# Performance work log

Measured on AMD Instinct MI355X. Metric: run time of the kernel, lower is better.

Reference implementation:

```python
import jax, jax.numpy as jnp
import numpy as np

EPS = 1e-6
DIM, HEADS, HEAD_DIM, FFN = 1024, 16, 64, 4096
B, S = 2, 2048


def layer_norm(x, g, b):
    m = jnp.mean(x, axis=-1, keepdims=True)
    v = jnp.mean(jnp.square(x - m), axis=-1, keepdims=True)
    return (x - m) * jax.lax.rsqrt(v + EPS) * g + b


def apply_rope(x, cos, sin):
    # x: (b, h, s, d); cos/sin: (s, d) broadcast over b, h
    x1, x2 = jnp.split(x, 2, axis=-1)
    rot = jnp.concatenate([-x2, x1], axis=-1)
    return x * cos + rot * sin


def setup_inputs() -> dict:
    key = jax.random.key(0)
    ks = jax.random.split(key, 24)
    sc_in = 1.0 / np.sqrt(DIM)
    sc_ffn = 1.0 / np.sqrt(FFN)
    inp = {
        "x": jax.random.normal(ks[0], (B, S, DIM), jnp.float32),
        "rope_cos": jax.random.uniform(ks[1], (S, HEAD_DIM), jnp.float32),
        "rope_sin": jax.random.uniform(ks[2], (S, HEAD_DIM), jnp.float32),
        "w_qkv": jax.random.normal(ks[3], (3 * DIM, DIM), jnp.float32) * sc_in,
        "b_qkv": jnp.zeros((3 * DIM,), jnp.float32),
        "w_out": jax.random.normal(ks[4], (DIM, DIM), jnp.float32) * sc_in,
        "b_out": jnp.zeros((DIM,), jnp.float32),
        "qn_g": jnp.ones((DIM,), jnp.float32),
        "qn_b": jnp.zeros((DIM,), jnp.float32),
        "kn_g": jnp.ones((DIM,), jnp.float32),
        "kn_b": jnp.zeros((DIM,), jnp.float32),
        "ln1_g": jnp.ones((DIM,), jnp.float32),
        "ln1_b": jnp.zeros((DIM,), jnp.float32),
        "ln2_g": jnp.ones((DIM,), jnp.float32),
        "ln2_b": jnp.zeros((DIM,), jnp.float32),
        "w1": jax.random.normal(ks[5], (FFN, DIM), jnp.float32) * sc_in,
        "b1": jnp.zeros((FFN,), jnp.float32),
        "w2": jax.random.normal(ks[6], (DIM, FFN), jnp.float32) * sc_ffn,
        "b2": jnp.zeros((DIM,), jnp.float32),
        "w3": jax.random.normal(ks[7], (FFN, DIM), jnp.float32) * sc_in,
        "b3": jnp.zeros((FFN,), jnp.float32),
    }
    return inp


def reference(x, rope_cos, rope_sin, w_qkv, b_qkv, w_out, b_out,
              qn_g, qn_b, kn_g, kn_b, ln1_g, ln1_b, ln2_g, ln2_b,
              w1, b1, w2, b2, w3, b3):
    bs, s, d = x.shape
    # --- pre-norm self-attention ---
    h = layer_norm(x, ln1_g, ln1_b)
    qkv = h @ w_qkv.T + b_qkv                      # (b, s, 3d)
    q, k, v = jnp.split(qkv, 3, axis=-1)
    q = layer_norm(q, qn_g, qn_b)                  # QK-norm over full dim
    k = layer_norm(k, kn_g, kn_b)
    # (b, s, d) -> (b, h, s, hd)
    q = q.reshape(bs, s, HEADS, HEAD_DIM).transpose(0, 2, 1, 3)
    k = k.reshape(bs, s, HEADS, HEAD_DIM).transpose(0, 2, 1, 3)
    v = v.reshape(bs, s, HEADS, HEAD_DIM).transpose(0, 2, 1, 3)
    q = apply_rope(q, rope_cos, rope_sin)
    k = apply_rope(k, rope_cos, rope_sin)
    scale = 1.0 / np.sqrt(HEAD_DIM)
    scores = jnp.einsum('bhqd,bhkd->bhqk', q, k) * scale
    probs = jax.nn.softmax(scores, axis=-1)
    attn = jnp.einsum('bhqk,bhkd->bhqd', probs, v)
    attn = attn.transpose(0, 2, 1, 3).reshape(bs, s, d)
    x = x + (attn @ w_out.T + b_out)
    # --- pre-norm SwiGLU FFN ---
    h2 = layer_norm(x, ln2_g, ln2_b)
    ffn = (jax.nn.silu(h2 @ w1.T + b1) * (h2 @ w3.T + b3)) @ w2.T + b2
    return x + ffn
```

## Files before the change

### kernel.cpp

```cpp
#include <hip/hip_runtime.h>
#include <hip/hip_bf16.h>


typedef __bf16 bf16_t;
typedef bf16_t bf16x8 __attribute__((ext_vector_type(8)));
typedef bf16_t bf16x4 __attribute__((ext_vector_type(4)));
typedef float  f32x4  __attribute__((ext_vector_type(4)));
typedef float  f32x16 __attribute__((ext_vector_type(16)));

#define DIM   1024
#define HEADS 16
#define HD    64
#define FFND  4096
#define NB    2
#define SEQ   2048
#define NTOK  (NB * SEQ)

#define GLOAD16(gp, lp) __builtin_amdgcn_global_load_lds( \
    (const __attribute__((address_space(1))) void*)(gp),  \
    (__attribute__((address_space(3))) void*)(lp), 16, 0, 0)

#define CVTPK(lo, hi_) ({ unsigned r_;                                        \
  asm("v_cvt_pk_bf16_f32 %0, %1, %2" : "=v"(r_) : "v"(lo), "v"(hi_)); r_; })
#define PLSWAP(a, b) asm("v_permlane32_swap_b32 %0, %1" : "+v"(a), "+v"(b))
#define SBAR() asm volatile("s_barrier" ::: "memory")

#define F2B_S0 786432
#define F2B_S1 262144
#define F2B_S2 1048576
#define F2B_S3 1048576
#define F2B_S4 1048576
#define F2B_C1 (F2B_S0)
#define F2B_C2 (F2B_C1 + F2B_S1)
#define F2B_C3 (F2B_C2 + F2B_S2)
#define F2B_C4 (F2B_C3 + F2B_S3)
#define F2B_N  (F2B_C4 + F2B_S4)

__global__ void f2bf_all_kernel(const float* __restrict__ s0, const float* __restrict__ s1,
                                const float* __restrict__ s2, const float* __restrict__ s3,
                                const float* __restrict__ s4,
                                bf16_t* __restrict__ d0, bf16_t* __restrict__ d1,
                                bf16_t* __restrict__ d2, bf16_t* __restrict__ d3,
                                bf16_t* __restrict__ d4) {
  int idx = blockIdx.x * blockDim.x + threadIdx.x;
  int stride = gridDim.x * blockDim.x;
  for (; idx < F2B_N; idx += stride) {
    const float* src; bf16_t* dst; int i;
    if (idx < F2B_C1)      { src = s0; dst = d0; i = idx; }
    else if (idx < F2B_C2) { src = s1; dst = d1; i = idx - F2B_C1; }
    else if (idx < F2B_C3) { src = s2; dst = d2; i = idx - F2B_C2; }
    else if (idx < F2B_C4) { src = s3; dst = d3; i = idx - F2B_C3; }
    else                   { src = s4; dst = d4; i = idx - F2B_C4; }
    float4 v = reinterpret_cast<const float4*>(src)[i];
    bf16x4 o;
    o[0] = (bf16_t)v.x; o[1] = (bf16_t)v.y; o[2] = (bf16_t)v.z; o[3] = (bf16_t)v.w;
    reinterpret_cast<bf16x4*>(dst)[i] = o;
  }
}

__global__ __launch_bounds__(256) void ln_kernel(
    const float* __restrict__ x, const float* __restrict__ g,
    const float* __restrict__ b, bf16_t* __restrict__ out) {
  int t = blockIdx.x;
  int i = threadIdx.x;
  float4 v = reinterpret_cast<const float4*>(x + (size_t)t * DIM)[i];
  float s  = v.x + v.y + v.z + v.w;
  float s2 = v.x * v.x + v.y * v.y + v.z * v.z + v.w * v.w;
#pragma unroll
  for (int off = 32; off > 0; off >>= 1) {
    s  += __shfl_down(s, off, 64);
    s2 += __shfl_down(s2, off, 64);
  }
  __shared__ float red[2][4];
  int wid = i >> 6, lane = i & 63;
  if (lane == 0) { red[0][wid] = s; red[1][wid] = s2; }
  __syncthreads();
  float S  = red[0][0] + red[0][1] + red[0][2] + red[0][3];
  float S2 = red[1][0] + red[1][1] + red[1][2] + red[1][3];
  float mean = S * (1.0f / DIM);
  float var  = S2 * (1.0f / DIM) - mean * mean;
  float r = rsqrtf(var + 1e-6f);
  float vv[4] = {v.x, v.y, v.z, v.w};
  bf16x4 o;
#pragma unroll
  for (int j = 0; j < 4; ++j) {
    int d = i * 4 + j;
    o[j] = (bf16_t)((vv[j] - mean) * r * g[d] + b[d]);
  }
  *reinterpret_cast<bf16x4*>(out + (size_t)t * DIM + i * 4) = o;
}

template <int OUT_MODE>
__global__ __launch_bounds__(512, 2) void gemm256(
    const bf16_t* __restrict__ A, const bf16_t* __restrict__ B,
    const float* __restrict__ bias, const bf16_t* __restrict__ comp,
    void* __restrict__ Cout, int M, int N, int Kfull, int Klen) {
  __shared__ __align__(16) bf16_t Al[2][256][64];
  __shared__ __align__(16) bf16_t Bl[2][256][64];
  const int nTn = N >> 8;
  const int nwg = gridDim.x;
  const int bid = blockIdx.x;
  const int swz = ((nwg & 7) == 0) ? ((bid & 7) * (nwg >> 3) + (bid >> 3)) : bid;
  const int bm = swz / nTn, bn = swz % nTn;
  const int k0base = blockIdx.z * Klen;
  const int NT = Klen >> 6;
  const int tid = threadIdx.x, wid = tid >> 6, lane = tid & 63;
  const int wm = wid >> 3, wn = wid & 3;
  const int wm2 = wid >> 2;
  (void)wm;
  const int lr = lane & 15, lg = lane >> 4;
  const int strow = wid * 8 + (lane >> 3);
  const int stg   = ((lane & 7) ^ ((lane >> 3) & 7)) << 3;
  const bf16_t* Abase = A + (size_t)(bm * 256 + strow) * Kfull + k0base + stg;
  const bf16_t* Bbase = B + (size_t)(bn * 256 + strow) * Kfull + k0base + stg;

#define STAGE_A(buf, half, c, t)                                              \
  GLOAD16(Abase + (size_t)((half) * 128 + (c) * 64) * Kfull + (t) * 64,       \
          &Al[buf][(half) * 128 + (c) * 64 + wid * 8][0])
#define STAGE_B(buf, half, c, t)                                              \
  GLOAD16(Bbase + (size_t)((half) * 128 + (c) * 64) * Kfull + (t) * 64,       \
          &Bl[buf][(half) * 128 + (c) * 64 + wid * 8][0])

  f32x4 acc[8][4] = {};
  STAGE_A(0, 0, 0, 0); STAGE_A(0, 0, 1, 0); STAGE_A(0, 1, 0, 0); STAGE_A(0, 1, 1, 0);
  STAGE_B(0, 0, 0, 0); STAGE_B(0, 0, 1, 0); STAGE_B(0, 1, 0, 0); STAGE_B(0, 1, 1, 0);

  for (int t = 0; t < NT; ++t) {
    const int cur = t & 1, nxt = cur ^ 1;
    const bool pf = (t + 1 < NT);
    if (pf) {
      STAGE_A(nxt, 0, 0, t + 1); STAGE_A(nxt, 0, 1, t + 1);
      STAGE_A(nxt, 1, 0, t + 1); STAGE_A(nxt, 1, 1, t + 1);
      asm volatile("s_waitcnt vmcnt(4)" ::: "memory");
    } else {
      asm volatile("s_waitcnt vmcnt(0)" ::: "memory");
    }
    SBAR();
    bf16x8 bfr[4][2], af[2][2];
#pragma unroll
    for (int nf = 0; nf < 4; ++nf)
#pragma unroll
      for (int ks = 0; ks < 2; ++ks) {
        const int row = wn * 64 + nf * 16 + lr;
        const int g = ((ks * 4 + lg) ^ (lane & 7)) << 3;
        bfr[nf][ks] = *reinterpret_cast<const bf16x8*>(&Bl[cur][row][g]);
      }
#pragma unroll
    for (int i = 0; i < 2; ++i)
#pragma unroll
      for (int ks = 0; ks < 2; ++ks) {
        const int row = wm2 * 128 + i * 16 + lr;
        const int g = ((ks * 4 + lg) ^ (lane & 7)) << 3;
        af[i][ks] = *reinterpret_cast<const bf16x8*>(&Al[cur][row][g]);
      }
    __builtin_amdgcn_s_setprio(1);
#pragma unroll
    for (int i = 0; i < 2; ++i)
#pragma unroll
      for (int nf = 0; nf < 4; ++nf)
#pragma unroll
        for (int ks = 0; ks < 2; ++ks)
          acc[i][nf] = __builtin_amdgcn_mfma_f32_16x16x32_bf16(af[i][ks], bfr[nf][ks], acc[i][nf], 0, 0, 0);
    __builtin_amdgcn_s_setprio(0);
    SBAR();
#pragma unroll
    for (int p = 1; p < 4; ++p) {
#pragma unroll
      for (int i = 0; i < 2; ++i)
#pragma unroll
        for (int ks = 0; ks < 2; ++ks) {
          const int row = wm2 * 128 + (p * 2 + i) * 16 + lr;
          const int g = ((ks * 4 + lg) ^ (lane & 7)) << 3;
          af[i][ks] = *reinterpret_cast<const bf16x8*>(&Al[cur][row][g]);
        }
      if (p == 1 && pf) {
        STAGE_B(nxt, 0, 0, t + 1); STAGE_B(nxt, 0, 1, t + 1);
        STAGE_B(nxt, 1, 0, t + 1); STAGE_B(nxt, 1, 1, t + 1);
      }
      SBAR();
      __builtin_amdgcn_s_setprio(1);
#pragma unroll
      for (int i = 0; i < 2; ++i)
#pragma unroll
        for (int nf = 0; nf < 4; ++nf)
#pragma unroll
          for (int ks = 0; ks < 2; ++ks)
            acc[p * 2 + i][nf] = __builtin_amdgcn_mfma_f32_16x16x32_bf16(af[i][ks], bfr[nf][ks], acc[p * 2 + i][nf], 0, 0, 0);
      __builtin_amdgcn_s_setprio(0);
      SBAR();
    }
  }
#undef STAGE_A
#undef STAGE_B
  const int r0 = lg * 4;
#pragma unroll
  for (int mf = 0; mf < 8; ++mf) {
#pragma unroll
    for (int r = 0; r < 4; ++r) {
      const int row = bm * 256 + wm2 * 128 + mf * 16 + r0 + r;
#pragma unroll
      for (int nf = 0; nf < 4; ++nf) {
        const int col = bn * 256 + wn * 64 + nf * 16 + lr;
        float v = acc[mf][nf][r];
        if (OUT_MODE == 1) {
          v += bias[col];
          reinterpret_cast<bf16_t*>(Cout)[(size_t)row * N + col] = (bf16_t)v;
        } else if (OUT_MODE == 2) {
          float* P = reinterpret_cast<float*>(Cout) + (size_t)blockIdx.z * M * N;
          P[(size_t)row * N + col] = v;
        } else {
          v += bias[col];
          float c1 = (float)comp[(size_t)row * N + col];
          float sg = c1 / (1.0f + __expf(-c1));
          reinterpret_cast<bf16_t*>(Cout)[(size_t)row * N + col] = (bf16_t)(sg * v);
        }
      }
    }
  }
}

__global__ void combine_kernel(const float* __restrict__ part,
                               const float* __restrict__ bias,
                               const float* __restrict__ res,
                               float* __restrict__ out, int n4) {
  const int slice = NTOK * DIM / 4;
  int i = blockIdx.x * blockDim.x + threadIdx.x;
  int stride = gridDim.x * blockDim.x;
  const float4* p = reinterpret_cast<const float4*>(part);
  const float4* r4 = reinterpret_cast<const float4*>(res);
  const float4* b4 = reinterpret_cast<const float4*>(bias);
  float4* o4 = reinterpret_cast<float4*>(out);
  for (; i < n4; i += stride) {
    float4 a = p[i], b = p[i + slice], c = p[i + 2 * slice], d = p[i + 3 * slice];
    float4 rr = r4[i];
    float4 bb = b4[i & 255];
    float4 o;
    o.x = a.x + b.x + c.x + d.x + bb.x + rr.x;
    o.y = a.y + b.y + c.y + d.y + bb.y + rr.y;
    o.z = a.z + b.z + c.z + d.z + bb.z + rr.z;
    o.w = a.w + b.w + c.w + d.w + bb.w + rr.w;
    o4[i] = o;
  }
}

template <int OUT_BF16, int HAS_RES>
__global__ __launch_bounds__(256) void gemm_bt(
    const bf16_t* __restrict__ A, const bf16_t* __restrict__ B,
    const float* __restrict__ bias, const float* __restrict__ res,
    void* __restrict__ Cout, int M, int N, int K) {
  __shared__ bf16_t As[128][32];
  __shared__ bf16_t Bs[128][32];
  const int nTn = N >> 7;
  const int bm = blockIdx.x / nTn;
  const int bn = blockIdx.x % nTn;
  const int tid  = threadIdx.x;
  const int wid  = tid >> 6;
  const int lane = tid & 63;
  const int wm = (wid >> 1) * 64, wn = (wid & 1) * 64;
  const int lr = lane & 15;
  const int gq = lane >> 4;
  const int sr = lane >> 2;
  const int sg = lane & 3;
  const int cS = ((sg ^ ((sr >> 1) & 3)) << 3);
  const int swg = ((gq ^ ((lr >> 1) & 3)) << 3);
  f32x4 acc[4][4] = {};
  const bf16_t* Ag0 = A + (size_t)(bm * 128 + wid * 16 + sr) * K + cS;
  const bf16_t* Ag1 = Ag0 + (size_t)64 * K;
  const bf16_t* Bg0 = B + (size_t)(bn * 128 + wid * 16 + sr) * K + cS;
  const bf16_t* Bg1 = Bg0 + (size_t)64 * K;
  bf16_t* ldsA0 = &As[wid * 16][0];
  bf16_t* ldsA1 = &As[64 + wid * 16][0];
  bf16_t* ldsB0 = &Bs[wid * 16][0];
  bf16_t* ldsB1 = &Bs[64 + wid * 16][0];
  for (int k0 = 0; k0 < K; k0 += 32) {
    __syncthreads();
    GLOAD16(Ag0 + k0, ldsA0);
    GLOAD16(Ag1 + k0, ldsA1);
    GLOAD16(Bg0 + k0, ldsB0);
    GLOAD16(Bg1 + k0, ldsB1);
    __syncthreads();
    bf16x8 af[4], bfr[4];
#pragma unroll
    for (int mi = 0; mi < 4; ++mi)
      af[mi] = *reinterpret_cast<const bf16x8*>(&As[wm + mi * 16 + lr][swg]);
#pragma unroll
    for (int ni = 0; ni < 4; ++ni)
      bfr[ni] = *reinterpret_cast<const bf16x8*>(&Bs[wn + ni * 16 + lr][swg]);
#pragma unroll
    for (int mi = 0; mi < 4; ++mi)
#pragma unroll
      for (int ni = 0; ni < 4; ++ni)
        acc[mi][ni] = __builtin_amdgcn_mfma_f32_16x16x32_bf16(af[mi], bfr[ni], acc[mi][ni], 0, 0, 0);
  }
  const int r0 = (lane >> 4) * 4;
#pragma unroll
  for (int mi = 0; mi < 4; ++mi) {
#pragma unroll
    for (int r = 0; r < 4; ++r) {
      int row = bm * 128 + wm + mi * 16 + r0 + r;
#pragma unroll
      for (int ni = 0; ni < 4; ++ni) {
        int col = bn * 128 + wn + ni * 16 + lr;
        float v = acc[mi][ni][r] + bias[col];
        if (HAS_RES) v += res[(size_t)row * N + col];
        if (OUT_BF16)
          reinterpret_cast<bf16_t*>(Cout)[(size_t)row * N + col] = (bf16_t)v;
        else
          reinterpret_cast<float*>(Cout)[(size_t)row * N + col] = v;
      }
    }
  }
}

__global__ __launch_bounds__(256) void qknorm_rope_kernel(
    const bf16_t* __restrict__ qkv,
    const float* __restrict__ qg, const float* __restrict__ qb,
    const float* __restrict__ kg, const float* __restrict__ kb,
    const float* __restrict__ rc, const float* __restrict__ rs,
    bf16_t* __restrict__ q_r, bf16_t* __restrict__ k_r) {
  int t = blockIdx.x;
  int b = t >> 11, s = t & 2047;
  const bf16_t* p = qkv + (size_t)t * 3072;
  int i = threadIdx.x;
  bf16x4 qv = *reinterpret_cast<const bf16x4*>(p + i * 4);
  bf16x4 kv = *reinterpret_cast<const bf16x4*>(p + 1024 + i * 4);
  float q4[4], k4[4];
  float sq = 0.f, sq2 = 0.f, sk = 0.f, sk2 = 0.f;
#pragma unroll
  for (int j = 0; j < 4; ++j) {
    q4[j] = (float)qv[j]; k4[j] = (float)kv[j];
    sq += q4[j]; sq2 += q4[j] * q4[j];
    sk += k4[j]; sk2 += k4[j] * k4[j];
  }
#pragma unroll
  for (int off = 32; off > 0; off >>= 1) {
    sq  += __shfl_down(sq, off, 64);
    sq2 += __shfl_down(sq2, off, 64);
    sk  += __shfl_down(sk, off, 64);
    sk2 += __shfl_down(sk2, off, 64);
  }
  __shared__ float red[4][4];
  int wid = i >> 6, lane = i & 63;
  if (lane == 0) { red[0][wid] = sq; red[1][wid] = sq2; red[2][wid] = sk; red[3][wid] = sk2; }
  __syncthreads();
  float Sq  = red[0][0] + red[0][1] + red[0][2] + red[0][3];
  float Sq2 = red[1][0] + red[1][1] + red[1][2] + red[1][3];
  float Sk  = red[2][0] + red[2][1] + red[2][2] + red[2][3];
  float Sk2 = red[3][0] + red[3][1] + red[3][2] + red[3][3];
  float mq = Sq * (1.0f / DIM);
  float vq = Sq2 * (1.0f / DIM) - mq * mq;
  float rq = rsqrtf(vq + 1e-6f);
  float mk = Sk * (1.0f / DIM);
  float vk = Sk2 * (1.0f / DIM) - mk * mk;
  float rk = rsqrtf(vk + 1e-6f);
  const float QS = 0.18033688011f;
#pragma unroll
  for (int j = 0; j < 4; ++j) {
    int d = i * 4 + j, h = d >> 6, hd = d & 63, dp = d ^ 32;
    float c  = rc[s * HD + hd];
    float sn = rs[s * HD + hd];
    float qn  = (q4[j] - mq) * rq * qg[d] + qb[d];
    float qpn = ((float)p[dp] - mq) * rq * qg[dp] + qb[dp];
    float qo  = qn * c + ((hd < 32) ? -qpn : qpn) * sn;
    float kn  = (k4[j] - mk) * rk * kg[d] + kb[d];
    float kpn = ((float)p[1024 + dp] - mk) * rk * kg[dp] + kb[dp];
    float ko  = kn * c + ((hd < 32) ? -kpn : kpn) * sn;
    size_t oi = ((size_t)(b * HEADS + h) * SEQ + s) * HD + hd;
    q_r[oi] = (bf16_t)(qo * QS);
    k_r[oi] = (bf16_t)ko;
  }
}

__global__ __launch_bounds__(256) void vtrans_kernel(
    const bf16_t* __restrict__ qkv, bf16_t* __restrict__ v_t) {
  __shared__ bf16_t T[64][72];
  const int st = blockIdx.x;
  const int bh = blockIdx.y;
  const int b = bh >> 4, h = bh & 15;
  const int tid = threadIdx.x;
  const int r = tid >> 2, c = (tid & 3) * 8;
  const bf16_t* src = qkv + (size_t)(b * SEQ + st * 64 + r) * 3072 + 2048 + h * 64;
  *reinterpret_cast<bf16x8*>(&T[r][c])      = *reinterpret_cast<const bf16x8*>(src + c);
  *reinterpret_cast<bf16x8*>(&T[r][c + 32]) = *reinterpret_cast<const bf16x8*>(src + c + 32);
  __syncthreads();
  bf16x8 o0, o1;
#pragma unroll
  for (int j = 0; j < 8; ++j) { o0[j] = T[c + j][r]; o1[j] = T[c + 32 + j][r]; }
  bf16_t* dst = v_t + ((size_t)bh * 64 + r) * SEQ + st * 64;
  *reinterpret_cast<bf16x8*>(dst + c)      = o0;
  *reinterpret_cast<bf16x8*>(dst + c + 32) = o1;
}

__global__ __launch_bounds__(512, 2) void attn_kernel(
    const bf16_t* __restrict__ q_r, const bf16_t* __restrict__ k_r,
    const bf16_t* __restrict__ v_t, bf16_t* __restrict__ attn_out) {
  __shared__ __align__(16) char smem[69632];
  bf16_t* KsB = (bf16_t*)smem;
  bf16_t* VsB = (bf16_t*)(smem + 32768);
  float*  Xch = (float*)smem;
  const int bid = blockIdx.x;
  const int hh = bid & 31;
  const int qt = bid >> 5;
  const int bidx = hh >> 4, h = hh & 15;
  const int tid = threadIdx.x, wid = tid >> 6, lane = tid & 63;
  const int kh = wid >> 2, ww = wid & 3;
  const int lq = lane & 31, hi = lane >> 5;
  const int qA = qt * 256 + ww * 64 + lq;
  const int qB = qA + 32;
  const bf16_t* Qp = q_r + (size_t)hh * SEQ * HD;
  const bf16_t* Kp = k_r + (size_t)hh * SEQ * HD + (size_t)kh * 1024 * HD;
  const bf16_t* Vp = v_t + (size_t)hh * HD * SEQ + kh * 1024;
  bf16_t* Ks0 = KsB + kh * 2 * 4096;
  bf16_t* Vs0 = VsB + kh * 2 * 4096;
  bf16x8 qfA[4], qfB[4];
#pragma unroll
  for (int kdt = 0; kdt < 4; ++kdt) {
    qfA[kdt] = *reinterpret_cast<const bf16x8*>(Qp + (size_t)qA * HD + kdt * 16 + hi * 8);
    qfB[kdt] = *reinterpret_cast<const bf16x8*>(Qp + (size_t)qB * HD + kdt * 16 + hi * 8);
  }
  f32x16 oA0 = {}, oA1 = {}, oB0 = {}, oB1 = {};
  float lA = 0.f, lB = 0.f;
  const int kSrcA = lane * HD + ww * 8;
  const int kSrcB = lane * HD + (ww + 4) * 8;
  const int vSrcA = lane * SEQ + ww * 8;
  const int vSrcB = lane * SEQ + (ww + 4) * 8;
  const int ldsA = ww * 512;
  const int ldsB = 2048 + ww * 512;
  GLOAD16(Kp + kSrcA, &Ks0[ldsA]);
  GLOAD16(Kp + kSrcB, &Ks0[ldsB]);
  GLOAD16(Vp + vSrcA, &Vs0[ldsA]);
  GLOAD16(Vp + vSrcB, &Vs0[ldsB]);
  __syncthreads();
  const int NT = 1024 / 64;
  for (int kt = 0; kt < NT; ++kt) {
    const int cur = kt & 1, nxt = cur ^ 1;
    if (kt + 1 < NT) {
      GLOAD16(Kp + (kt + 1) * (64 * HD) + kSrcA, &Ks0[nxt * 4096 + ldsA]);
      GLOAD16(Kp + (kt + 1) * (64 * HD) + kSrcB, &Ks0[nxt * 4096 + ldsB]);
      GLOAD16(Vp + (kt + 1) * 64 + vSrcA, &Vs0[nxt * 4096 + ldsA]);
      GLOAD16(Vp + (kt + 1) * 64 + vSrcB, &Vs0[nxt * 4096 + ldsB]);
    }
    f32x16 sA0 = {}, sA1 = {}, sB0 = {}, sB1 = {};
#pragma unroll
    for (int kdt = 0; kdt < 4; ++kdt) {
      const int goff = cur * 4096 + (kdt * 2 + hi) * 512;
      bf16x8 kf0 = *reinterpret_cast<const bf16x8*>(&Ks0[goff + lq * 8]);
      bf16x8 kf1 = *reinterpret_cast<const bf16x8*>(&Ks0[goff + (lq + 32) * 8]);
      sA0 = __builtin_amdgcn_mfma_f32_32x32x16_bf16(kf0, qfA[kdt], sA0, 0, 0, 0);
      sA1 = __builtin_amdgcn_mfma_f32_32x32x16_bf16(kf1, qfA[kdt], sA1, 0, 0, 0);
      sB0 = __builtin_amdgcn_mfma_f32_32x32x16_bf16(kf0, qfB[kdt], sB0, 0, 0, 0);
      sB1 = __builtin_amdgcn_mfma_f32_32x32x16_bf16(kf1, qfB[kdt], sB1, 0, 0, 0);
    }
#pragma unroll
    for (int i = 0; i < 16; ++i) sA0[i] = __builtin_amdgcn_exp2f(sA0[i]);
#pragma unroll
    for (int i = 0; i < 16; ++i) sA1[i] = __builtin_amdgcn_exp2f(sA1[i]);
#pragma unroll
    for (int i = 0; i < 16; ++i) sB0[i] = __builtin_amdgcn_exp2f(sB0[i]);
#pragma unroll
    for (int i = 0; i < 16; ++i) sB1[i] = __builtin_amdgcn_exp2f(sB1[i]);
    {
      f32x16 t = sA0 + sA1;
      float a = ((t[0] + t[8]) + (t[4] + t[12])) + ((t[2] + t[10]) + (t[6] + t[14]));
      float b = ((t[1] + t[9]) + (t[5] + t[13])) + ((t[3] + t[11]) + (t[7] + t[15]));
      lA += a + b;
      f32x16 u = sB0 + sB1;
      float c = ((u[0] + u[8]) + (u[4] + u[12])) + ((u[2] + u[10]) + (u[6] + u[14]));
      float d = ((u[1] + u[9]) + (u[5] + u[13])) + ((u[3] + u[11]) + (u[7] + u[15]));
      lB += c + d;
    }
#pragma unroll
    for (int tt = 0; tt < 2; ++tt) {
#pragma unroll
      for (int ks = 0; ks < 2; ++ks) {
        const f32x16& pA = tt ? sA1 : sA0;
        const f32x16& pB = tt ? sB1 : sB0;
        unsigned a0, b0, c0, d0, a1, b1, c1, d1;
        if (ks == 0) {
          a0 = CVTPK(pA[0], pA[1]); b0 = CVTPK(pA[4], pA[5]);
          c0 = CVTPK(pA[2], pA[3]); d0 = CVTPK(pA[6], pA[7]);
          a1 = CVTPK(pB[0], pB[1]); b1 = CVTPK(pB[4], pB[5]);
          c1 = CVTPK(pB[2], pB[3]); d1 = CVTPK(pB[6], pB[7]);
        } else {
          a0 = CVTPK(pA[8], pA[9]);   b0 = CVTPK(pA[12], pA[13]);
          c0 = CVTPK(pA[10], pA[11]); d0 = CVTPK(pA[14], pA[15]);
          a1 = CVTPK(pB[8], pB[9]);   b1 = CVTPK(pB[12], pB[13]);
          c1 = CVTPK(pB[10], pB[11]); d1 = CVTPK(pB[14], pB[15]);
        }
        PLSWAP(a0, b0); PLSWAP(c0, d0); PLSWAP(a1, b1); PLSWAP(c1, d1);
        union { unsigned u[4]; bf16x8 v; } pfA, pfB;
        pfA.u[0] = a0; pfA.u[1] = c0; pfA.u[2] = b0; pfA.u[3] = d0;
        pfB.u[0] = a1; pfB.u[1] = c1; pfB.u[2] = b1; pfB.u[3] = d1;
        const int gv = cur * 4096 + (tt * 4 + ks * 2 + hi) * 512;
        bf16x8 vf0 = *reinterpret_cast<const bf16x8*>(&Vs0[gv + lq * 8]);
        bf16x8 vf1 = *reinterpret_cast<const bf16x8*>(&Vs0[gv + (lq + 32) * 8]);
        oA0 = __builtin_amdgcn_mfma_f32_32x32x16_bf16(vf0, pfA.v, oA0, 0, 0, 0);
        oA1 = __builtin_amdgcn_mfma_f32_32x32x16_bf16(vf1, pfA.v, oA1, 0, 0, 0);
        oB0 = __builtin_amdgcn_mfma_f32_32x32x16_bf16(vf0, pfB.v, oB0, 0, 0, 0);
        oB1 = __builtin_amdgcn_mfma_f32_32x32x16_bf16(vf1, pfB.v, oB1, 0, 0, 0);
      }
    }
    __syncthreads();
  }
  lA += __shfl_xor(lA, 32, 64);
  lB += __shfl_xor(lB, 32, 64);
  if (kh == 1) {
    float* my = Xch + (size_t)(ww * 64 + lane) * 68;
#pragma unroll
    for (int g = 0; g < 4; ++g) {
      *reinterpret_cast<float4*>(my + g * 4)      = make_float4(oA0[g*4], oA0[g*4+1], oA0[g*4+2], oA0[g*4+3]);
      *reinterpret_cast<float4*>(my + 16 + g * 4) = make_float4(oA1[g*4], oA1[g*4+1], oA1[g*4+2], oA1[g*4+3]);
      *reinterpret_cast<float4*>(my + 32 + g * 4) = make_float4(oB0[g*4], oB0[g*4+1], oB0[g*4+2], oB0[g*4+3]);
      *reinterpret_cast<float4*>(my + 48 + g * 4) = make_float4(oB1[g*4], oB1[g*4+1], oB1[g*4+2], oB1[g*4+3]);
    }
    my[64] = lA; my[65] = lB;
  }
  __syncthreads();
  if (kh == 0) {
    const float* pr = Xch + (size_t)(ww * 64 + lane) * 68;
#pragma unroll
    for (int i = 0; i < 16; ++i) {
      oA0[i] += pr[i];      oA1[i] += pr[16 + i];
      oB0[i] += pr[32 + i]; oB1[i] += pr[48 + i];
    }
    float invA = 1.0f / (lA + pr[64]);
    float invB = 1.0f / (lB + pr[65]);
    bf16_t* orowA = attn_out + ((size_t)(bidx * SEQ + qA)) * DIM + h * 64;
    bf16_t* orowB = attn_out + ((size_t)(bidx * SEQ + qB)) * DIM + h * 64;
#pragma unroll
    for (int g = 0; g < 4; ++g) {
      bf16x4 wA0, wA1, wB0, wB1;
#pragma unroll
      for (int j = 0; j < 4; ++j) {
        wA0[j] = (bf16_t)(oA0[g * 4 + j] * invA);
        wA1[j] = (bf16_t)(oA1[g * 4 + j] * invA);
        wB0[j] = (bf16_t)(oB0[g * 4 + j] * invB);
        wB1[j] = (bf16_t)(oB1[g * 4 + j] * invB);
      }
      *reinterpret_cast<bf16x4*>(orowA + g * 8 + 4 * hi)      = wA0;
      *reinterpret_cast<bf16x4*>(orowA + 32 + g * 8 + 4 * hi) = wA1;
      *reinterpret_cast<bf16x4*>(orowB + g * 8 + 4 * hi)      = wB0;
      *reinterpret_cast<bf16x4*>(orowB + 32 + g * 8 + 4 * hi) = wB1;
    }
  }
}

extern "C" void kernel_launch(void* const* d_in, const int* in_sizes, int n_in,
                              void* d_out, int out_size, void* d_ws, size_t ws_size,
                              hipStream_t stream) {
  const float* x        = (const float*)d_in[0];
  const float* rope_cos = (const float*)d_in[1];
  const float* rope_sin = (const float*)d_in[2];
  const float* w_qkv    = (const float*)d_in[3];
  const float* b_qkv    = (const float*)d_in[4];
  const float* w_out    = (const float*)d_in[5];
  const float* b_out    = (const float*)d_in[6];
  const float* qn_g     = (const float*)d_in[7];
  const float* qn_b     = (const float*)d_in[8];
  const float* kn_g     = (const float*)d_in[9];
  const float* kn_b     = (const float*)d_in[10];
  const float* ln1_g    = (const float*)d_in[11];
  const float* ln1_b    = (const float*)d_in[12];
  const float* ln2_g    = (const float*)d_in[13];
  const float* ln2_b    = (const float*)d_in[14];
  const float* w1       = (const float*)d_in[15];
  const float* b1       = (const float*)d_in[16];
  const float* w2       = (const float*)d_in[17];
  const float* b2       = (const float*)d_in[18];
  const float* w3       = (const float*)d_in[19];
  const float* b3       = (const float*)d_in[20];

  const size_t OFF_WQKV = 0;
  const size_t OFF_WOUT = 6291456;
  const size_t OFF_W1   = 8388608;
  const size_t OFF_W2   = 16777216;
  const size_t OFF_W3   = 25165824;
  const size_t OFF_H1   = 33554432;
  const size_t OFF_QKV  = 41943040;
  const size_t OFF_QR   = 67108864;
  const size_t OFF_KR   = 75497472;
  const size_t OFF_VT   = 83886080;
  const size_t OFF_ATT  = 92274688;
  const size_t OFF_X2   = 100663296;
  const size_t OFF_H2   = 117440512;
  const size_t OFF_A1   = 33554432;
  const size_t OFF_A3   = 67108864;
  const size_t OFF_PART = 125829120;
  const size_t NEEDED   = 125829120;
  const size_t NEED_SPLIT = OFF_PART + 67108864;
  if (ws_size < NEEDED) return;
  const bool use_split = (ws_size >= NEED_SPLIT);

  char* ws = (char*)d_ws;
  bf16_t* wqkv_bf = (bf16_t*)(ws + OFF_WQKV);
  bf16_t* wout_bf = (bf16_t*)(ws + OFF_WOUT);
  bf16_t* w1_bf   = (bf16_t*)(ws + OFF_W1);
  bf16_t* w2_bf   = (bf16_t*)(ws + OFF_W2);
  bf16_t* w3_bf   = (bf16_t*)(ws + OFF_W3);
  bf16_t* h1      = (bf16_t*)(ws + OFF_H1);
  bf16_t* qkv     = (bf16_t*)(ws + OFF_QKV);
  bf16_t* q_r     = (bf16_t*)(ws + OFF_QR);
  bf16_t* k_r     = (bf16_t*)(ws + OFF_KR);
  bf16_t* v_t     = (bf16_t*)(ws + OFF_VT);
  bf16_t* att     = (bf16_t*)(ws + OFF_ATT);
  float*  x2      = (float*)(ws + OFF_X2);
  bf16_t* h2      = (bf16_t*)(ws + OFF_H2);
  bf16_t* a1      = (bf16_t*)(ws + OFF_A1);
  bf16_t* a3      = (bf16_t*)(ws + OFF_A3);
  float*  part    = (float*)(ws + OFF_PART);
  float*  out     = (float*)d_out;

  f2bf_all_kernel<<<2048, 256, 0, stream>>>(w_qkv, w_out, w1, w2, w3,
                                            wqkv_bf, wout_bf, w1_bf, w2_bf, w3_bf);
  ln_kernel<<<NTOK, 256, 0, stream>>>(x, ln1_g, ln1_b, h1);
  gemm256<1><<<dim3(192, 1, 1), 512, 0, stream>>>(h1, wqkv_bf, b_qkv, nullptr, qkv,
                                                  NTOK, 3072, DIM, DIM);
  qknorm_rope_kernel<<<NTOK, 256, 0, stream>>>(qkv, qn_g, qn_b, kn_g, kn_b,
                                               rope_cos, rope_sin, q_r, k_r);
  vtrans_kernel<<<dim3(SEQ / 64, NB * HEADS), 256, 0, stream>>>(qkv, v_t);
  attn_kernel<<<256, 512, 0, stream>>>(q_r, k_r, v_t, att);
  gemm_bt<0, 1><<<32 * 8, 256, 0, stream>>>(att, wout_bf, b_out, x, x2, NTOK, DIM, DIM);
  ln_kernel<<<NTOK, 256, 0, stream>>>(x2, ln2_g, ln2_b, h2);
  gemm256<1><<<dim3(256, 1, 1), 512, 0, stream>>>(h2, w1_bf, b1, nullptr, a1,
                                                  NTOK, FFND, DIM, DIM);
  gemm256<3><<<dim3(256, 1, 1), 512, 0, stream>>>(h2, w3_bf, b3, a1, a3,
                                                  NTOK, FFND, DIM, DIM);
  if (use_split) {
    gemm256<2><<<dim3(64, 1, 4), 512, 0, stream>>>(a3, w2_bf, nullptr, nullptr, part,
                                                   NTOK, DIM, FFND, FFND / 4);
    combine_kernel<<<2048, 256, 0, stream>>>(part, b2, x2, out, NTOK * DIM / 4);
  } else {
    gemm_bt<0, 1><<<32 * 8, 256, 0, stream>>>(a3, w2_bf, b2, x2, out, NTOK, DIM, FFND);
  }
}
```

Before: 320.8 us.

## Replace 256x256 pipelined GEMM with unified 128x128 single-buffered GEMM kernel

```diff
diff --git a/kernel.cpp b/kernel.cpp
--- a/kernel.cpp
+++ b/kernel.cpp
@@ -23,7 +23,6 @@
 #define CVTPK(lo, hi_) ({ unsigned r_;                                        \
   asm("v_cvt_pk_bf16_f32 %0, %1, %2" : "=v"(r_) : "v"(lo), "v"(hi_)); r_; })
 #define PLSWAP(a, b) asm("v_permlane32_swap_b32 %0, %1" : "+v"(a), "+v"(b))
-#define SBAR() asm volatile("s_barrier" ::: "memory")
 
 #define F2B_S0 786432
 #define F2B_S1 262144
@@ -91,118 +90,73 @@
 }
 
 template <int OUT_MODE>
-__global__ __launch_bounds__(512, 2) void gemm256(
+__global__ __launch_bounds__(256) void gemm_bt(
     const bf16_t* __restrict__ A, const bf16_t* __restrict__ B,
-    const float* __restrict__ bias, const bf16_t* __restrict__ comp,
-    void* __restrict__ Cout, int M, int N, int Kfull, int Klen) {
-  __shared__ __align__(16) bf16_t Al[2][256][64];
-  __shared__ __align__(16) bf16_t Bl[2][256][64];
-  const int nTn = N >> 8;
+    const float* __restrict__ bias, const float* __restrict__ res,
+    const bf16_t* __restrict__ comp, void* __restrict__ Cout,
+    int M, int N, int Kfull, int Klen) {
+  __shared__ bf16_t As[128][32];
+  __shared__ bf16_t Bs[128][32];
+  const int nTn = N >> 7;
   const int nwg = gridDim.x;
   const int bid = blockIdx.x;
   const int swz = ((nwg & 7) == 0) ? ((bid & 7) * (nwg >> 3) + (bid >> 3)) : bid;
-  const int bm = swz / nTn, bn = swz % nTn;
+  const int bm = swz / nTn;
+  const int bn = swz % nTn;
   const int k0base = blockIdx.z * Klen;
-  const int NT = Klen >> 6;
-  const int tid = threadIdx.x, wid = tid >> 6, lane = tid & 63;
-  const int wm = wid >> 3, wn = wid & 3;
-  const int wm2 = wid >> 2;
-  (void)wm;
-  const int lr = lane & 15, lg = lane >> 4;
-  const int strow = wid * 8 + (lane >> 3);
-  const int stg   = ((lane & 7) ^ ((lane >> 3) & 7)) << 3;
-  const bf16_t* Abase = A + (size_t)(bm * 256 + strow) * Kfull + k0base + stg;
-  const bf16_t* Bbase = B + (size_t)(bn * 256 + strow) * Kfull + k0base + stg;
-
-#define STAGE_A(buf, half, c, t)                                              \
-  GLOAD16(Abase + (size_t)((half) * 128 + (c) * 64) * Kfull + (t) * 64,       \
-          &Al[buf][(half) * 128 + (c) * 64 + wid * 8][0])
-#define STAGE_B(buf, half, c, t)                                              \
-  GLOAD16(Bbase + (size_t)((half) * 128 + (c) * 64) * Kfull + (t) * 64,       \
-          &Bl[buf][(half) * 128 + (c) * 64 + wid * 8][0])
-
-  f32x4 acc[8][4] = {};
-  STAGE_A(0, 0, 0, 0); STAGE_A(0, 0, 1, 0); STAGE_A(0, 1, 0, 0); STAGE_A(0, 1, 1, 0);
-  STAGE_B(0, 0, 0, 0); STAGE_B(0, 0, 1, 0); STAGE_B(0, 1, 0, 0); STAGE_B(0, 1, 1, 0);
-
-  for (int t = 0; t < NT; ++t) {
-    const int cur = t & 1, nxt = cur ^ 1;
-    const bool pf = (t + 1 < NT);
-    if (pf) {
-      STAGE_A(nxt, 0, 0, t + 1); STAGE_A(nxt, 0, 1, t + 1);
-      STAGE_A(nxt, 1, 0, t + 1); STAGE_A(nxt, 1, 1, t + 1);
-      asm volatile("s_waitcnt vmcnt(4)" ::: "memory");
-    } else {
-      asm volatile("s_waitcnt vmcnt(0)" ::: "memory");
-    }
-    SBAR();
-    bf16x8 bfr[4][2], af[2][2];
-#pragma unroll
-    for (int nf = 0; nf < 4; ++nf)
-#pragma unroll
-      for (int ks = 0; ks < 2; ++ks) {
-        const int row = wn * 64 + nf * 16 + lr;
-        const int g = ((ks * 4 + lg) ^ (lane & 7)) << 3;
-        bfr[nf][ks] = *reinterpret_cast<const bf16x8*>(&Bl[cur][row][g]);
-      }
-#pragma unroll
-    for (int i = 0; i < 2; ++i)
-#pragma unroll
-      for (int ks = 0; ks < 2; ++ks) {
-        const int row = wm2 * 128 + i * 16 + lr;
-        const int g = ((ks * 4 + lg) ^ (lane & 7)) << 3;
-        af[i][ks] = *reinterpret_cast<const bf16x8*>(&Al[cur][row][g]);
-      }
-    __builtin_amdgcn_s_setprio(1);
-#pragma unroll
-    for (int i = 0; i < 2; ++i)
-#pragma unroll
-      for (int nf = 0; nf < 4; ++nf)
-#pragma unroll
-        for (int ks = 0; ks < 2; ++ks)
-          acc[i][nf] = __builtin_amdgcn_mfma_f32_16x16x32_bf16(af[i][ks], bfr[nf][ks], acc[i][nf], 0, 0, 0);
-    __builtin_amdgcn_s_setprio(0);
-    SBAR();
-#pragma unroll
-    for (int p = 1; p < 4; ++p) {
-#pragma unroll
-      for (int i = 0; i < 2; ++i)
-#pragma unroll
-        for (int ks = 0; ks < 2; ++ks) {
-          const int row = wm2 * 128 + (p * 2 + i) * 16 + lr;
-          const int g = ((ks * 4 + lg) ^ (lane & 7)) << 3;
-          af[i][ks] = *reinterpret_cast<const bf16x8*>(&Al[cur][row][g]);
-        }
-      if (p == 1 && pf) {
-        STAGE_B(nxt, 0, 0, t + 1); STAGE_B(nxt, 0, 1, t + 1);
-        STAGE_B(nxt, 1, 0, t + 1); STAGE_B(nxt, 1, 1, t + 1);
-      }
-      SBAR();
-      __builtin_amdgcn_s_setprio(1);
-#pragma unroll
-      for (int i = 0; i < 2; ++i)
-#pragma unroll
-        for (int nf = 0; nf < 4; ++nf)
-#pragma unroll
-          for (int ks = 0; ks < 2; ++ks)
-            acc[p * 2 + i][nf] = __builtin_amdgcn_mfma_f32_16x16x32_bf16(af[i][ks], bfr[nf][ks], acc[p * 2 + i][nf], 0, 0, 0);
-      __builtin_amdgcn_s_setprio(0);
-      SBAR();
-    }
-  }
-#undef STAGE_A
-#undef STAGE_B
-  const int r0 = lg * 4;
-#pragma unroll
-  for (int mf = 0; mf < 8; ++mf) {
+  const int tid  = threadIdx.x;
+  const int wid  = tid >> 6;
+  const int lane = tid & 63;
+  const int wm = (wid >> 1) * 64, wn = (wid & 1) * 64;
+  const int lr = lane & 15;
+  const int gq = lane >> 4;
+  const int sr = lane >> 2;
+  const int sg = lane & 3;
+  const int cS = ((sg ^ ((sr >> 1) & 3)) << 3);
+  const int swg = ((gq ^ ((lr >> 1) & 3)) << 3);
+  f32x4 acc[4][4] = {};
+  const bf16_t* Ag0 = A + (size_t)(bm * 128 + wid * 16 + sr) * Kfull + k0base + cS;
+  const bf16_t* Ag1 = Ag0 + (size_t)64 * Kfull;
+  const bf16_t* Bg0 = B + (size_t)(bn * 128 + wid * 16 + sr) * Kfull + k0base + cS;
+  const bf16_t* Bg1 = Bg0 + (size_t)64 * Kfull;
+  bf16_t* ldsA0 = &As[wid * 16][0];
+  bf16_t* ldsA1 = &As[64 + wid * 16][0];
+  bf16_t* ldsB0 = &Bs[wid * 16][0];
+  bf16_t* ldsB1 = &Bs[64 + wid * 16][0];
+  for (int k0 = 0; k0 < Klen; k0 += 32) {
+    __syncthreads();
+    GLOAD16(Ag0 + k0, ldsA0);
+    GLOAD16(Ag1 + k0, ldsA1);
+    GLOAD16(Bg0 + k0, ldsB0);
+    GLOAD16(Bg1 + k0, ldsB1);
+    __syncthreads();
+    bf16x8 af[4], bfr[4];
+#pragma unroll
+    for (int mi = 0; mi < 4; ++mi)
+      af[mi] = *reinterpret_cast<const bf16x8*>(&As[wm + mi * 16 + lr][swg]);
+#pragma unroll
+    for (int ni = 0; ni < 4; ++ni)
+      bfr[ni] = *reinterpret_cast<const bf16x8*>(&Bs[wn + ni * 16 + lr][swg]);
+#pragma unroll
+    for (int mi = 0; mi < 4; ++mi)
+#pragma unroll
+      for (int ni = 0; ni < 4; ++ni)
+        acc[mi][ni] = __builtin_amdgcn_mfma_f32_16x16x32_bf16(af[mi], bfr[ni], acc[mi][ni], 0, 0, 0);
+  }
+  const int r0 = (lane >> 4) * 4;
+#pragma unroll
+  for (int mi = 0; mi < 4; ++mi) {
 #pragma unroll
     for (int r = 0; r < 4; ++r) {
-      const int row = bm * 256 + wm2 * 128 + mf * 16 + r0 + r;
-#pragma unroll
-      for (int nf = 0; nf < 4; ++nf) {
-        const int col = bn * 256 + wn * 64 + nf * 16 + lr;
-        float v = acc[mf][nf][r];
-        if (OUT_MODE == 1) {
+      int row = bm * 128 + wm + mi * 16 + r0 + r;
+#pragma unroll
+      for (int ni = 0; ni < 4; ++ni) {
+        int col = bn * 128 + wn + ni * 16 + lr;
+        float v = acc[mi][ni][r];
+        if (OUT_MODE == 0) {
+          v += bias[col] + res[(size_t)row * N + col];
+          reinterpret_cast<float*>(Cout)[(size_t)row * N + col] = v;
+        } else if (OUT_MODE == 1) {
           v += bias[col];
           reinterpret_cast<bf16_t*>(Cout)[(size_t)row * N + col] = (bf16_t)v;
         } else if (OUT_MODE == 2) {
@@ -211,8 +165,8 @@
         } else {
           v += bias[col];
           float c1 = (float)comp[(size_t)row * N + col];
-          float sg = c1 / (1.0f + __expf(-c1));
-          reinterpret_cast<bf16_t*>(Cout)[(size_t)row * N + col] = (bf16_t)(sg * v);
+          float sg_ = c1 / (1.0f + __expf(-c1));
+          reinterpret_cast<bf16_t*>(Cout)[(size_t)row * N + col] = (bf16_t)(sg_ * v);
         }
       }
     }
@@ -240,75 +194,6 @@
     o.z = a.z + b.z + c.z + d.z + bb.z + rr.z;
     o.w = a.w + b.w + c.w + d.w + bb.w + rr.w;
     o4[i] = o;
-  }
-}
-
-template <int OUT_BF16, int HAS_RES>
-__global__ __launch_bounds__(256) void gemm_bt(
-    const bf16_t* __restrict__ A, const bf16_t* __restrict__ B,
-    const float* __restrict__ bias, const float* __restrict__ res,
-    void* __restrict__ Cout, int M, int N, int K) {
-  __shared__ bf16_t As[128][32];
-  __shared__ bf16_t Bs[128][32];
-  const int nTn = N >> 7;
-  const int bm = blockIdx.x / nTn;
-  const int bn = blockIdx.x % nTn;
-  const int tid  = threadIdx.x;
-  const int wid  = tid >> 6;
-  const int lane = tid & 63;
-  const int wm = (wid >> 1) * 64, wn = (wid & 1) * 64;
-  const int lr = lane & 15;
-  const int gq = lane >> 4;
-  const int sr = lane >> 2;
-  const int sg = lane & 3;
-  const int cS = ((sg ^ ((sr >> 1) & 3)) << 3);
-  const int swg = ((gq ^ ((lr >> 1) & 3)) << 3);
-  f32x4 acc[4][4] = {};
-  const bf16_t* Ag0 = A + (size_t)(bm * 128 + wid * 16 + sr) * K + cS;
-  const bf16_t* Ag1 = Ag0 + (size_t)64 * K;
-  const bf16_t* Bg0 = B + (size_t)(bn * 128 + wid * 16 + sr) * K + cS;
-  const bf16_t* Bg1 = Bg0 + (size_t)64 * K;
-  bf16_t* ldsA0 = &As[wid * 16][0];
-  bf16_t* ldsA1 = &As[64 + wid * 16][0];
-  bf16_t* ldsB0 = &Bs[wid * 16][0];
-  bf16_t* ldsB1 = &Bs[64 + wid * 16][0];
-  for (int k0 = 0; k0 < K; k0 += 32) {
-    __syncthreads();
-    GLOAD16(Ag0 + k0, ldsA0);
-    GLOAD16(Ag1 + k0, ldsA1);
-    GLOAD16(Bg0 + k0, ldsB0);
-    GLOAD16(Bg1 + k0, ldsB1);
-    __syncthreads();
-    bf16x8 af[4], bfr[4];
-#pragma unroll
-    for (int mi = 0; mi < 4; ++mi)
-      af[mi] = *reinterpret_cast<const bf16x8*>(&As[wm + mi * 16 + lr][swg]);
-#pragma unroll
-    for (int ni = 0; ni < 4; ++ni)
-      bfr[ni] = *reinterpret_cast<const bf16x8*>(&Bs[wn + ni * 16 + lr][swg]);
-#pragma unroll
-    for (int mi = 0; mi < 4; ++mi)
-#pragma unroll
-      for (int ni = 0; ni < 4; ++ni)
-        acc[mi][ni] = __builtin_amdgcn_mfma_f32_16x16x32_bf16(af[mi], bfr[ni], acc[mi][ni], 0, 0, 0);
-  }
-  const int r0 = (lane >> 4) * 4;
-#pragma unroll
-  for (int mi = 0; mi < 4; ++mi) {
-#pragma unroll
-    for (int r = 0; r < 4; ++r) {
-      int row = bm * 128 + wm + mi * 16 + r0 + r;
-#pragma unroll
-      for (int ni = 0; ni < 4; ++ni) {
-        int col = bn * 128 + wn + ni * 16 + lr;
-        float v = acc[mi][ni][r] + bias[col];
-        if (HAS_RES) v += res[(size_t)row * N + col];
-        if (OUT_BF16)
-          reinterpret_cast<bf16_t*>(Cout)[(size_t)row * N + col] = (bf16_t)v;
-        else
-          reinterpret_cast<float*>(Cout)[(size_t)row * N + col] = v;
-      }
-    }
   }
 }
 
@@ -613,23 +498,31 @@
   f2bf_all_kernel<<<2048, 256, 0, stream>>>(w_qkv, w_out, w1, w2, w3,
                                             wqkv_bf, wout_bf, w1_bf, w2_bf, w3_bf);
   ln_kernel<<<NTOK, 256, 0, stream>>>(x, ln1_g, ln1_b, h1);
-  gemm256<1><<<dim3(192, 1, 1), 512, 0, stream>>>(h1, wqkv_bf, b_qkv, nullptr, qkv,
-                                                  NTOK, 3072, DIM, DIM);
+  gemm_bt<1><<<dim3(32 * 24, 1, 1), 256, 0, stream>>>(
+      h1, wqkv_bf, b_qkv, nullptr, nullptr, qkv, NTOK, 3072, DIM, DIM);
   qknorm_rope_kernel<<<NTOK, 256, 0, stream>>>(qkv, qn_g, qn_b, kn_g, kn_b,
                                                rope_cos, rope_sin, q_r, k_r);
   vtrans_kernel<<<dim3(SEQ / 64, NB * HEADS), 256, 0, stream>>>(qkv, v_t);
   attn_kernel<<<256, 512, 0, stream>>>(q_r, k_r, v_t, att);
-  gemm_bt<0, 1><<<32 * 8, 256, 0, stream>>>(att, wout_bf, b_out, x, x2, NTOK, DIM, DIM);
+  if (use_split) {
+    gemm_bt<2><<<dim3(32 * 8, 1, 4), 256, 0, stream>>>(
+        att, wout_bf, nullptr, nullptr, nullptr, part, NTOK, DIM, DIM, DIM / 4);
+    combine_kernel<<<2048, 256, 0, stream>>>(part, b_out, x, x2, NTOK * DIM / 4);
+  } else {
+    gemm_bt<0><<<dim3(32 * 8, 1, 1), 256, 0, stream>>>(
+        att, wout_bf, b_out, x, nullptr, x2, NTOK, DIM, DIM, DIM);
+  }
   ln_kernel<<<NTOK, 256, 0, stream>>>(x2, ln2_g, ln2_b, h2);
-  gemm256<1><<<dim3(256, 1, 1), 512, 0, stream>>>(h2, w1_bf, b1, nullptr, a1,
-                                                  NTOK, FFND, DIM, DIM);
-  gemm256<3><<<dim3(256, 1, 1), 512, 0, stream>>>(h2, w3_bf, b3, a1, a3,
-                                                  NTOK, FFND, DIM, DIM);
+  gemm_bt<1><<<dim3(32 * 32, 1, 1), 256, 0, stream>>>(
+      h2, w1_bf, b1, nullptr, nullptr, a1, NTOK, FFND, DIM, DIM);
+  gemm_bt<3><<<dim3(32 * 32, 1, 1), 256, 0, stream>>>(
+      h2, w3_bf, b3, nullptr, a1, a3, NTOK, FFND, DIM, DIM);
   if (use_split) {
-    gemm256<2><<<dim3(64, 1, 4), 512, 0, stream>>>(a3, w2_bf, nullptr, nullptr, part,
-                                                   NTOK, DIM, FFND, FFND / 4);
+    gemm_bt<2><<<dim3(32 * 8, 1, 4), 256, 0, stream>>>(
+        a3, w2_bf, nullptr, nullptr, nullptr, part, NTOK, DIM, FFND, FFND / 4);
     combine_kernel<<<2048, 256, 0, stream>>>(part, b2, x2, out, NTOK * DIM / 4);
   } else {
-    gemm_bt<0, 1><<<32 * 8, 256, 0, stream>>>(a3, w2_bf, b2, x2, out, NTOK, DIM, FFND);
-  }
-}
+    gemm_bt<0><<<dim3(32 * 8, 1, 1), 256, 0, stream>>>(
+        a3, w2_bf, b2, x2, nullptr, out, NTOK, DIM, FFND, FFND);
+  }
+}
```

After: 357.9 us. +11.6%, slower.

## Simplify gemm256 main loop to single barrier with full-tile fragment loads

Applied to the files above, without the earlier changes.

```diff
diff --git a/kernel.cpp b/kernel.cpp
--- a/kernel.cpp
+++ b/kernel.cpp
@@ -105,9 +105,7 @@
   const int k0base = blockIdx.z * Klen;
   const int NT = Klen >> 6;
   const int tid = threadIdx.x, wid = tid >> 6, lane = tid & 63;
-  const int wm = wid >> 3, wn = wid & 3;
-  const int wm2 = wid >> 2;
-  (void)wm;
+  const int wm2 = wid >> 2, wn = wid & 3;
   const int lr = lane & 15, lg = lane >> 4;
   const int strow = wid * 8 + (lane >> 3);
   const int stg   = ((lane & 7) ^ ((lane >> 3) & 7)) << 3;
@@ -127,67 +125,36 @@
 
   for (int t = 0; t < NT; ++t) {
     const int cur = t & 1, nxt = cur ^ 1;
-    const bool pf = (t + 1 < NT);
-    if (pf) {
+    asm volatile("s_waitcnt vmcnt(0)" ::: "memory");
+    SBAR();
+    if (t + 1 < NT) {
       STAGE_A(nxt, 0, 0, t + 1); STAGE_A(nxt, 0, 1, t + 1);
       STAGE_A(nxt, 1, 0, t + 1); STAGE_A(nxt, 1, 1, t + 1);
-      asm volatile("s_waitcnt vmcnt(4)" ::: "memory");
-    } else {
-      asm volatile("s_waitcnt vmcnt(0)" ::: "memory");
-    }
-    SBAR();
-    bf16x8 bfr[4][2], af[2][2];
-#pragma unroll
-    for (int nf = 0; nf < 4; ++nf)
-#pragma unroll
-      for (int ks = 0; ks < 2; ++ks) {
+      STAGE_B(nxt, 0, 0, t + 1); STAGE_B(nxt, 0, 1, t + 1);
+      STAGE_B(nxt, 1, 0, t + 1); STAGE_B(nxt, 1, 1, t + 1);
+    }
+#pragma unroll
+    for (int ks = 0; ks < 2; ++ks) {
+      bf16x8 af[8], bfr[4];
+#pragma unroll
+      for (int nf = 0; nf < 4; ++nf) {
         const int row = wn * 64 + nf * 16 + lr;
         const int g = ((ks * 4 + lg) ^ (lane & 7)) << 3;
-        bfr[nf][ks] = *reinterpret_cast<const bf16x8*>(&Bl[cur][row][g]);
+        bfr[nf] = *reinterpret_cast<const bf16x8*>(&Bl[cur][row][g]);
       }
 #pragma unroll
-    for (int i = 0; i < 2; ++i)
-#pragma unroll
-      for (int ks = 0; ks < 2; ++ks) {
-        const int row = wm2 * 128 + i * 16 + lr;
+      for (int mf = 0; mf < 8; ++mf) {
+        const int row = wm2 * 128 + mf * 16 + lr;
         const int g = ((ks * 4 + lg) ^ (lane & 7)) << 3;
-        af[i][ks] = *reinterpret_cast<const bf16x8*>(&Al[cur][row][g]);
+        af[mf] = *reinterpret_cast<const bf16x8*>(&Al[cur][row][g]);
       }
-    __builtin_amdgcn_s_setprio(1);
-#pragma unroll
-    for (int i = 0; i < 2; ++i)
-#pragma unroll
-      for (int nf = 0; nf < 4; ++nf)
-#pragma unroll
-        for (int ks = 0; ks < 2; ++ks)
-          acc[i][nf] = __builtin_amdgcn_mfma_f32_16x16x32_bf16(af[i][ks], bfr[nf][ks], acc[i][nf], 0, 0, 0);
-    __builtin_amdgcn_s_setprio(0);
-    SBAR();
-#pragma unroll
-    for (int p = 1; p < 4; ++p) {
-#pragma unroll
-      for (int i = 0; i < 2; ++i)
-#pragma unroll
-        for (int ks = 0; ks < 2; ++ks) {
-          const int row = wm2 * 128 + (p * 2 + i) * 16 + lr;
-          const int g = ((ks * 4 + lg) ^ (lane & 7)) << 3;
-          af[i][ks] = *reinterpret_cast<const bf16x8*>(&Al[cur][row][g]);
-        }
-      if (p == 1 && pf) {
-        STAGE_B(nxt, 0, 0, t + 1); STAGE_B(nxt, 0, 1, t + 1);
-        STAGE_B(nxt, 1, 0, t + 1); STAGE_B(nxt, 1, 1, t + 1);
-      }
-      SBAR();
       __builtin_amdgcn_s_setprio(1);
 #pragma unroll
-      for (int i = 0; i < 2; ++i)
+      for (int mf = 0; mf < 8; ++mf)
 #pragma unroll
         for (int nf = 0; nf < 4; ++nf)
-#pragma unroll
-          for (int ks = 0; ks < 2; ++ks)
-            acc[p * 2 + i][nf] = __builtin_amdgcn_mfma_f32_16x16x32_bf16(af[i][ks], bfr[nf][ks], acc[p * 2 + i][nf], 0, 0, 0);
+          acc[mf][nf] = __builtin_amdgcn_mfma_f32_16x16x32_bf16(af[mf], bfr[nf], acc[mf][nf], 0, 0, 0);
       __builtin_amdgcn_s_setprio(0);
-      SBAR();
     }
   }
 #undef STAGE_A
@@ -243,16 +210,20 @@
   }
 }
 
-template <int OUT_BF16, int HAS_RES>
+template <int OUT_MODE>
 __global__ __launch_bounds__(256) void gemm_bt(
     const bf16_t* __restrict__ A, const bf16_t* __restrict__ B,
     const float* __restrict__ bias, const float* __restrict__ res,
-    void* __restrict__ Cout, int M, int N, int K) {
+    void* __restrict__ Cout, int M, int N, int Kfull, int Klen) {
   __shared__ bf16_t As[128][32];
   __shared__ bf16_t Bs[128][32];
   const int nTn = N >> 7;
-  const int bm = blockIdx.x / nTn;
-  const int bn = blockIdx.x % nTn;
+  const int nwg = gridDim.x;
+  const int bid = blockIdx.x;
+  const int swz = ((nwg & 7) == 0) ? ((bid & 7) * (nwg >> 3) + (bid >> 3)) : bid;
+  const int bm = swz / nTn;
+  const int bn = swz % nTn;
+  const int k0base = blockIdx.z * Klen;
   const int tid  = threadIdx.x;
   const int wid  = tid >> 6;
   const int lane = tid & 63;
@@ -264,15 +235,15 @@
   const int cS = ((sg ^ ((sr >> 1) & 3)) << 3);
   const int swg = ((gq ^ ((lr >> 1) & 3)) << 3);
   f32x4 acc[4][4] = {};
-  const bf16_t* Ag0 = A + (size_t)(bm * 128 + wid * 16 + sr) * K + cS;
-  const bf16_t* Ag1 = Ag0 + (size_t)64 * K;
-  const bf16_t* Bg0 = B + (size_t)(bn * 128 + wid * 16 + sr) * K + cS;
-  const bf16_t* Bg1 = Bg0 + (size_t)64 * K;
+  const bf16_t* Ag0 = A + (size_t)(bm * 128 + wid * 16 + sr) * Kfull + k0base + cS;
+  const bf16_t* Ag1 = Ag0 + (size_t)64 * Kfull;
+  const bf16_t* Bg0 = B + (size_t)(bn * 128 + wid * 16 + sr) * Kfull + k0base + cS;
+  const bf16_t* Bg1 = Bg0 + (size_t)64 * Kfull;
   bf16_t* ldsA0 = &As[wid * 16][0];
   bf16_t* ldsA1 = &As[64 + wid * 16][0];
   bf16_t* ldsB0 = &Bs[wid * 16][0];
   bf16_t* ldsB1 = &Bs[64 + wid * 16][0];
-  for (int k0 = 0; k0 < K; k0 += 32) {
+  for (int k0 = 0; k0 < Klen; k0 += 32) {
     __syncthreads();
     GLOAD16(Ag0 + k0, ldsA0);
     GLOAD16(Ag1 + k0, ldsA1);
@@ -301,12 +272,14 @@
 #pragma unroll
       for (int ni = 0; ni < 4; ++ni) {
         int col = bn * 128 + wn + ni * 16 + lr;
-        float v = acc[mi][ni][r] + bias[col];
-        if (HAS_RES) v += res[(size_t)row * N + col];
-        if (OUT_BF16)
-          reinterpret_cast<bf16_t*>(Cout)[(size_t)row * N + col] = (bf16_t)v;
-        else
+        float v = acc[mi][ni][r];
+        if (OUT_MODE == 0) {
+          v += bias[col] + res[(size_t)row * N + col];
           reinterpret_cast<float*>(Cout)[(size_t)row * N + col] = v;
+        } else {
+          float* P = reinterpret_cast<float*>(Cout) + (size_t)blockIdx.z * M * N;
+          P[(size_t)row * N + col] = v;
+        }
       }
     }
   }
@@ -619,7 +592,8 @@
                                                rope_cos, rope_sin, q_r, k_r);
   vtrans_kernel<<<dim3(SEQ / 64, NB * HEADS), 256, 0, stream>>>(qkv, v_t);
   attn_kernel<<<256, 512, 0, stream>>>(q_r, k_r, v_t, att);
-  gemm_bt<0, 1><<<32 * 8, 256, 0, stream>>>(att, wout_bf, b_out, x, x2, NTOK, DIM, DIM);
+  gemm_bt<0><<<dim3(32 * 8, 1, 1), 256, 0, stream>>>(
+      att, wout_bf, b_out, x, x2, NTOK, DIM, DIM, DIM);
   ln_kernel<<<NTOK, 256, 0, stream>>>(x2, ln2_g, ln2_b, h2);
   gemm256<1><<<dim3(256, 1, 1), 512, 0, stream>>>(h2, w1_bf, b1, nullptr, a1,
                                                   NTOK, FFND, DIM, DIM);
@@ -630,6 +604,7 @@
                                                    NTOK, DIM, FFND, FFND / 4);
     combine_kernel<<<2048, 256, 0, stream>>>(part, b2, x2, out, NTOK * DIM / 4);
   } else {
-    gemm_bt<0, 1><<<32 * 8, 256, 0, stream>>>(a3, w2_bf, b2, x2, out, NTOK, DIM, FFND);
-  }
-}
+    gemm_bt<0><<<dim3(32 * 8, 1, 1), 256, 0, stream>>>(
+        a3, w2_bf, b2, x2, out, NTOK, DIM, FFND, FFND);
+  }
+}
```

New measurement: 298.8 us. 1.07x faster.
